# Kernel tuning notes

Measured on AMD Instinct MI355X. Metric: run time of the kernel, lower is better.

## Reference

```python
import jax, jax.numpy as jnp
import numpy as np

K, S, P = 3, 2, 2  # kernel_size, stride, padding (dilation=1)


def _unfold(xp, k, s, oh, ow):
    """Extract k*k strided patches from a padded array.

    xp: (..., Hp, Wp) -> (..., k*k, oh, ow), window-position ordering (kh, kw)
    matching torch.nn.Unfold (channel-major handled by caller).
    """
    return jnp.stack(
        [xp[..., i:i + s * (oh - 1) + 1:s, j:j + s * (ow - 1) + 1:s]
         for i in range(K) for j in range(K)],
        axis=-3,
    )


def setup_inputs() -> dict:
    key = jax.random.key(0)
    x = jax.random.normal(key, (8, 256, 128, 128), dtype=jnp.float32)
    return {"x": x}


def reference(x):
    b, c, h, w = x.shape
    oh = (h - K + 2 * P) // S + 1
    ow = (w - K + 2 * P) // S + 1

    # channel-wise L2 norm, computed BEFORE unfolding (padding contributes 0 either way)
    n = jnp.sqrt(jnp.sum(x * x, axis=1))            # (b, h, w)
    n_pad = jnp.pad(n, ((0, 0), (P, P), (P, P)))
    n_patch = _unfold(n_pad, K, S, oh, ow)          # (b, k*k, oh, ow)
    # weighting_fn = softmax over the k*k window positions (torch dim=1 of unfolded norm)
    wts = jax.nn.softmax(n_patch, axis=1)           # (b, k*k, oh, ow)

    x_pad = jnp.pad(x, ((0, 0), (0, 0), (P, P), (P, P)))
    x_patch = _unfold(x_pad, K, S, oh, ow)          # (b, c, k*k, oh, ow)

    # weighted sum over window positions
    return jnp.sum(wts[:, None] * x_patch, axis=2)  # (b, c, oh, ow)
```

## Files before the change

kernel.cpp:

```cpp
#include <hip/hip_runtime.h>
#include <math.h>

#define BATCH 8
#define CH    256
#define H     128
#define W     128
#define HW    (H * W)
#define OH    65
#define OW    65
#define NPIX  (OH * OW)

__global__ __launch_bounds__(512, 4) void fused_kernel(const float* __restrict__ x,
                                                       float* __restrict__ out) {
    __shared__ float nrm[3][W];
    __shared__ float wts[OW][9];
    const int oh   = blockIdx.x;
    const int b    = blockIdx.y;
    const int t    = threadIdx.x;
    const int lane = t & 63;
    const int wv   = t >> 6;

    if (t < 3 * W) {
        const int r   = t >> 7;
        const int col = t & (W - 1);
        const int ih  = 2 * oh + r - 2;
        float s = 0.f;
        if ((unsigned)ih < (unsigned)H) {
            const float* p = x + (size_t)b * CH * HW + ih * W + col;
            float acc = 0.f;
            #pragma unroll 8
            for (int c = 0; c < CH; ++c) {
                float v = p[(size_t)c * HW];
                acc += v * v;
            }
            s = sqrtf(acc);
        }
        nrm[r][col] = s;
    }
    __syncthreads();

    if (t < OW) {
        const int iw0 = 2 * t - 2;
        float ww[9];
        bool  vl[9];
        float m = 0.f;
        #pragma unroll
        for (int r = 0; r < 3; ++r) {
            int ih = 2 * oh + r - 2;
            bool vh = (unsigned)ih < (unsigned)H;
            #pragma unroll
            for (int kw = 0; kw < 3; ++kw) {
                int iw = iw0 + kw;
                bool v = vh && ((unsigned)iw < (unsigned)W);
                int iwc = iw < 0 ? 0 : (iw > W - 1 ? W - 1 : iw);
                float nv = v ? nrm[r][iwc] : 0.f;
                vl[r * 3 + kw] = v;
                ww[r * 3 + kw] = nv;
                m = fmaxf(m, nv);
            }
        }
        float d = 0.f;
        #pragma unroll
        for (int k = 0; k < 9; ++k) {
            float e = __expf(ww[k] - m);
            d += e;
            ww[k] = vl[k] ? e : 0.f;
        }
        float inv = 1.f / d;
        #pragma unroll
        for (int k = 0; k < 9; ++k) wts[t][k] = ww[k] * inv;
    }
    __syncthreads();

    float w0[9], w64[9];
    #pragma unroll
    for (int k = 0; k < 9; ++k) { w0[k] = wts[lane][k]; w64[k] = wts[OW - 1][k]; }

    int rb[3];
    #pragma unroll
    for (int r = 0; r < 3; ++r) {
        int ih = 2 * oh + r - 2;
        int ihc = ih < 0 ? 0 : (ih > H - 1 ? H - 1 : ih);
        rb[r] = ihc * W;
    }

    const float* xb = x + (size_t)(b * CH + wv * 32) * HW;
    float*       ob = out + (size_t)(b * CH + wv * 32) * NPIX + oh * OW;

    #pragma unroll 4
    for (int c = 0; c < 32; ++c) {
        const float* xc = xb + (size_t)c * HW;
        float2 own[3], prev[3];
        #pragma unroll
        for (int r = 0; r < 3; ++r)
            own[r] = *(const float2*)(xc + rb[r] + 2 * lane);
        #pragma unroll
        for (int r = 0; r < 3; ++r) {
            prev[r].x = __shfl_up(own[r].x, 1);
            prev[r].y = __shfl_up(own[r].y, 1);
        }
        float a0 = 0.f, a1 = 0.f;
        #pragma unroll
        for (int r = 0; r < 3; ++r) {
            a0 += w0[r * 3 + 0] * prev[r].x + w0[r * 3 + 1] * prev[r].y
                + w0[r * 3 + 2] * own[r].x;
            a1 += w64[r * 3 + 0] * own[r].x + w64[r * 3 + 1] * own[r].y;
        }
        float* oc = ob + (size_t)c * NPIX;
        oc[lane] = a0;
        if (lane == 63) oc[OW - 1] = a1;
    }
}

extern "C" void kernel_launch(void* const* d_in, const int* in_sizes, int n_in,
                              void* d_out, int out_size, void* d_ws, size_t ws_size,
                              hipStream_t stream) {
    const float* x = (const float*)d_in[0];
    float* out = (float*)d_out;
    dim3 grid(OH, BATCH);
    fused_kernel<<<grid, 512, 0, stream>>>(x, out);
}
```

Measured before the change: 232.6 us.

## Parallelize channel-norm reduction across all waves with float4 loads and LDS partials

The norm phase used to run on 384 threads, each looping serially over all 256 channels with scalar strided loads. Now all 8 waves each reduce a 32-channel slice of three contiguous rows using float4 loads, write partial sums to shared memory, and 384 threads then add the 8 partials and take the square root. Rows are indexed relative to a clamped base row so the three loaded rows are always in bounds. This spreads the serial channel loop across more threads and memory-level parallelism, at the cost of an extra shared buffer and barrier, and it loads rows that the padding later masks out at the edges.

```diff
diff --git a/kernel.cpp b/kernel.cpp
--- a/kernel.cpp
+++ b/kernel.cpp
@@ -12,7 +12,8 @@
 
 __global__ __launch_bounds__(512, 4) void fused_kernel(const float* __restrict__ x,
                                                        float* __restrict__ out) {
-    __shared__ float nrm[3][W];
+    __shared__ float part[8][384];
+    __shared__ float nrmabs[3][W];
     __shared__ float wts[OW][9];
     const int oh   = blockIdx.x;
     const int b    = blockIdx.y;
@@ -20,22 +21,37 @@
     const int lane = t & 63;
     const int wv   = t >> 6;
 
-    if (t < 3 * W) {
-        const int r   = t >> 7;
-        const int col = t & (W - 1);
-        const int ih  = 2 * oh + r - 2;
+    const int ih0  = 2 * oh - 2;
+    int base = ih0 < 0 ? 0 : ih0;
+    if (base > H - 3) base = H - 3;
+
+    {
+        const float* xw = x + (size_t)(b * CH + wv * 32) * HW + base * W;
+        float4 a0 = {0.f, 0.f, 0.f, 0.f};
+        float4 a1 = {0.f, 0.f, 0.f, 0.f};
+        #pragma unroll 4
+        for (int c = 0; c < 32; ++c) {
+            const float4* p4 = (const float4*)(xw + (size_t)c * HW);
+            float4 v0 = p4[lane];
+            a0.x += v0.x * v0.x; a0.y += v0.y * v0.y;
+            a0.z += v0.z * v0.z; a0.w += v0.w * v0.w;
+            if (lane < 32) {
+                float4 v1 = p4[64 + lane];
+                a1.x += v1.x * v1.x; a1.y += v1.y * v1.y;
+                a1.z += v1.z * v1.z; a1.w += v1.w * v1.w;
+            }
+        }
+        float4* prow = (float4*)part[wv];
+        prow[lane] = a0;
+        if (lane < 32) prow[64 + lane] = a1;
+    }
+    __syncthreads();
+
+    if (t < 384) {
         float s = 0.f;
-        if ((unsigned)ih < (unsigned)H) {
-            const float* p = x + (size_t)b * CH * HW + ih * W + col;
-            float acc = 0.f;
-            #pragma unroll 8
-            for (int c = 0; c < CH; ++c) {
-                float v = p[(size_t)c * HW];
-                acc += v * v;
-            }
-            s = sqrtf(acc);
-        }
-        nrm[r][col] = s;
+        #pragma unroll
+        for (int w = 0; w < 8; ++w) s += part[w][t];
+        nrmabs[t >> 7][t & 127] = sqrtf(s);
     }
     __syncthreads();
 
@@ -46,14 +62,15 @@
         float m = 0.f;
         #pragma unroll
         for (int r = 0; r < 3; ++r) {
-            int ih = 2 * oh + r - 2;
+            int ih = ih0 + r;
             bool vh = (unsigned)ih < (unsigned)H;
+            int slot = vh ? (ih - base) : 0;
             #pragma unroll
             for (int kw = 0; kw < 3; ++kw) {
                 int iw = iw0 + kw;
                 bool v = vh && ((unsigned)iw < (unsigned)W);
                 int iwc = iw < 0 ? 0 : (iw > W - 1 ? W - 1 : iw);
-                float nv = v ? nrm[r][iwc] : 0.f;
+                float nv = v ? nrmabs[slot][iwc] : 0.f;
                 vl[r * 3 + kw] = v;
                 ww[r * 3 + kw] = nv;
                 m = fmaxf(m, nv);
@@ -79,7 +96,7 @@
     int rb[3];
     #pragma unroll
     for (int r = 0; r < 3; ++r) {
-        int ih = 2 * oh + r - 2;
+        int ih = ih0 + r;
         int ihc = ih < 0 ? 0 : (ih > H - 1 ? H - 1 : ih);
         rb[r] = ihc * W;
     }
```

Result: no change. 236.4 us (+1.6%).
